# Kernel tuning notes

Hardware: AMD Instinct MI355X
Metric: run time of the kernel (lower is better)

## Reference

```python
import jax, jax.numpy as jnp
import numpy as np

N, T, H, W, C = 4, 8, 64, 64, 512
WS = 8  # window size; H, W are exact multiples so pad/depad are identity


def setup_inputs() -> dict:
    key = jax.random.key(0)
    k1, k2, k3, k4 = jax.random.split(key, 4)
    x = jax.random.normal(k1, (N, T, H, W, C), dtype=jnp.float32)
    local_pos_embed = jax.random.normal(k2, (WS, WS, C), dtype=jnp.float32)
    W_in = jax.random.normal(k3, (3 * C, C), dtype=jnp.float32) * 0.02
    b_in = jnp.zeros((3 * C,), dtype=jnp.float32)
    W_out = jax.random.normal(k4, (C, C), dtype=jnp.float32) * 0.02
    b_out = jnp.zeros((C,), dtype=jnp.float32)
    return {"x": x, "local_pos_embed": local_pos_embed, "W_in": W_in,
            "b_in": b_in, "W_out": W_out, "b_out": b_out, "num_heads": 8}


def reference(x, local_pos_embed, W_in, b_in, W_out, b_out, num_heads):
    n, t, h, w, c = x.shape
    ws = local_pos_embed.shape[0]
    nh, nw = h // ws, w // ws
    head_dim = c // num_heads
    scale = 1.0 / jnp.sqrt(jnp.asarray(head_dim, dtype=x.dtype))

    # window partition: (N*T, H, W, C) -> (N*T*nh*nw, ws*ws, C)
    xw = x.reshape(n * t, nh, ws, nw, ws, c)
    xw = xw.transpose(0, 1, 3, 2, 4, 5).reshape(n * t * nh * nw, ws * ws, c)

    pos = local_pos_embed.reshape(ws * ws, c)  # flatten(0,1)
    qk_in = xw + pos[None, :, :]               # pos added to q,k only

    Wq, Wk, Wv = W_in[:c], W_in[c:2 * c], W_in[2 * c:]
    bq, bk, bv = b_in[:c], b_in[c:2 * c], b_in[2 * c:]

    B, S = qk_in.shape[0], qk_in.shape[1]
    q = (qk_in @ Wq.T + bq).reshape(B, S, num_heads, head_dim)
    k = (qk_in @ Wk.T + bk).reshape(B, S, num_heads, head_dim)
    v = (xw @ Wv.T + bv).reshape(B, S, num_heads, head_dim)

    scores = jnp.einsum('bqhd,bkhd->bhqk', q * scale, k)
    attn = jax.nn.softmax(scores, axis=-1)
    out = jnp.einsum('bhqk,bkhd->bqhd', attn, v).reshape(B, S, c)
    out = out @ W_out.T + b_out

    # reverse window partition
    out = out.reshape(n * t, nh, nw, ws, ws, c)
    out = out.transpose(0, 1, 3, 2, 4, 5).reshape(n, t, h, w, c)
    return out
```

## Files before the change

kernel.cpp:

```cpp
#include <hip/hip_runtime.h>

typedef _Float16 f16;
typedef unsigned int u32;
typedef f16 f16x8 __attribute__((ext_vector_type(8)));
typedef f16 f16x4 __attribute__((ext_vector_type(4)));
typedef float f32x4 __attribute__((ext_vector_type(4)));


__device__ __forceinline__ int src_row(int m) {
    int win = m >> 6, s = m & 63;
    return ((win >> 6) << 12) | (((win >> 3) & 7) << 9) | ((s >> 3) << 6) |
           ((win & 7) << 3) | (s & 7);
}

__device__ __forceinline__ void gload_lds16(const void* g, void* lds) {
    __builtin_amdgcn_global_load_lds(
        (const __attribute__((address_space(1))) u32*)g,
        (__attribute__((address_space(3))) u32*)lds, 16, 0, 0);
}

__global__ __launch_bounds__(256) void prep_weights_k(
        const float* __restrict__ Wi, const float* __restrict__ Wo,
        f16* __restrict__ Wi_h, f16* __restrict__ Wo_h) {
    int i = blockIdx.x * 256 + threadIdx.x;
    const float4* src;
    f16* dst;
    int idx;
    if (i < 196608) { src = (const float4*)Wi; dst = Wi_h; idx = i; }
    else            { src = (const float4*)Wo; dst = Wo_h; idx = i - 196608; }
    float4 v = src[idx];
    f16x4 h = {(f16)v.x, (f16)v.y, (f16)v.z, (f16)v.w};
    *(f16x4*)(dst + (size_t)idx * 4) = h;
}

__global__ __launch_bounds__(256) void prep_bias_k(
        const float* __restrict__ pos, const float* __restrict__ Wi,
        const float* __restrict__ b_in, float* __restrict__ biasT) {
    int idx = blockIdx.x * 256 + threadIdx.x;
    int s = idx / 1536, o = idx % 1536;
    float acc = b_in[o];
    if (o < 1024) {
        const float4* p4 = (const float4*)(pos + (size_t)s * 512);
        const float4* w4 = (const float4*)(Wi + (size_t)o * 512);
        #pragma unroll 4
        for (int c = 0; c < 128; ++c) {
            float4 a = p4[c], b = w4[c];
            acc += a.x * b.x + a.y * b.y + a.z * b.z + a.w * b.w;
        }
    }
    biasT[idx] = acc;
}

__global__ __launch_bounds__(256) void prep_x_k(
        const float* __restrict__ x, f16* __restrict__ xh, int m0) {
    int i = blockIdx.x * 256 + threadIdx.x;
    int ml = i >> 6, c8 = (i & 63) * 8;
    int sr = src_row(m0 + ml);
    const float4* s4 = (const float4*)(x + (size_t)sr * 512 + c8);
    float4 a = s4[0], b = s4[1];
    f16x8 hv = {(f16)a.x, (f16)a.y, (f16)a.z, (f16)a.w,
                (f16)b.x, (f16)b.y, (f16)b.z, (f16)b.w};
    *(f16x8*)(xh + (size_t)ml * 512 + c8) = hv;
}

__global__ void __launch_bounds__(512, 2) qkv_gemm8_k(
        const f16* __restrict__ xh, const f16* __restrict__ Wh,
        const float* __restrict__ biasT, f16* __restrict__ qk,
        f16* __restrict__ vT, int nblk) {
    extern __shared__ f16 lds[];
    int tid = threadIdx.x;
    int lane = tid & 63, wid = tid >> 6;
    int l15 = lane & 15, g = lane >> 4;
    int wm = wid >> 2, wn = wid & 3;
    int sid = (blockIdx.x & 7) * (nblk >> 3) + (blockIdx.x >> 3);
    int bm = sid / 6, bn = sid % 6;
    const f16* Ap = xh + (size_t)bm * 256 * 512;
    const f16* Bp = Wh + (size_t)bn * 256 * 512;

    int li0 = tid, li1 = tid + 512;
    int r0 = li0 >> 3, c0 = li0 & 7, r1 = li1 >> 3, c1 = li1 & 7;
    int off0 = r0 * 512 + ((c0 ^ (r0 & 7)) * 8);
    int off1 = r1 * 512 + ((c1 ^ (r1 & 7)) * 8);

    auto stage = [&](const f16* panel, int ldsbase, int tt, int h) {
        int tb = tt & 1;
        int dst = ldsbase + (tb * 2 + h) * 8192 + wid * 512;
        const f16* src = panel + h * 65536 + tt * 64;
        gload_lds16(src + off0, (void*)&lds[dst]);
        gload_lds16(src + off1, (void*)&lds[dst + 4096]);
    };

    f32x4 acc[8][4];
    f32x4 zero4 = {0.f, 0.f, 0.f, 0.f};
    #pragma unroll
    for (int a = 0; a < 8; ++a)
        #pragma unroll
        for (int b = 0; b < 4; ++b) acc[a][b] = zero4;
    f16x8 bf[4][2];

    stage(Ap, 0, 0, 0); stage(Ap, 0, 0, 1);
    stage(Bp, 32768, 0, 0); stage(Bp, 32768, 0, 1);
    stage(Ap, 0, 1, 0); stage(Ap, 0, 1, 1);
    stage(Bp, 32768, 1, 0); stage(Bp, 32768, 1, 1);
    asm volatile("s_waitcnt vmcnt(0)" ::: "memory");
    __builtin_amdgcn_s_barrier();

    #pragma unroll
    for (int tt = 0; tt < 8; ++tt) {
        int tb = tt & 1;
        const f16* Ab = &lds[(tb * 2 + wm) * 8192];
        const f16* Bb = &lds[32768 + (tb * 2 + (wn >> 1)) * 8192];
        #pragma unroll
        for (int q = 0; q < 4; ++q) {
            f16x8 af[2][2];
            #pragma unroll
            for (int ml = 0; ml < 2; ++ml) {
                int rr = (q * 2 + ml) * 16 + l15;
                #pragma unroll
                for (int ks = 0; ks < 2; ++ks)
                    af[ml][ks] = *(const f16x8*)&Ab[rr * 64 + (((ks * 4 + g) ^ (rr & 7)) * 8)];
            }
            if (q == 0) {
                #pragma unroll
                for (int nf = 0; nf < 4; ++nf) {
                    int rb = (wn & 1) * 64 + nf * 16 + l15;
                    #pragma unroll
                    for (int ks = 0; ks < 2; ++ks)
                        bf[nf][ks] = *(const f16x8*)&Bb[rb * 64 + (((ks * 4 + g) ^ (rb & 7)) * 8)];
                }
            }
            if (q <= 1) {
                if ((tt & 1) ? (tt + 1 < 8) : (tt >= 2)) stage(Ap, 0, tt + 1, q);
            } else {
                if (tt + 2 < 8) stage(Bp, 32768, tt + 2, q - 2);
            }
            __builtin_amdgcn_s_barrier();
            __builtin_amdgcn_s_setprio(1);
            #pragma unroll
            for (int ml = 0; ml < 2; ++ml)
                #pragma unroll
                for (int nf = 0; nf < 4; ++nf)
                    #pragma unroll
                    for (int ks = 0; ks < 2; ++ks)
                        acc[q * 2 + ml][nf] = __builtin_amdgcn_mfma_f32_16x16x32_f16(
                            af[ml][ks], bf[nf][ks], acc[q * 2 + ml][nf], 0, 0, 0);
            __builtin_amdgcn_s_setprio(0);
            if (q == 3) {
                if (tt < 6)       asm volatile("s_waitcnt vmcnt(4)" ::: "memory");
                else if (tt == 6) asm volatile("s_waitcnt vmcnt(0)" ::: "memory");
            }
            __builtin_amdgcn_s_barrier();
        }
    }

    int browg = bm * 256 + wm * 128;
    if (bn < 4) {
        #pragma unroll
        for (int mf = 0; mf < 8; ++mf) {
            #pragma unroll
            for (int nf = 0; nf < 4; ++nf) {
                int col = bn * 256 + wn * 64 + nf * 16 + l15;
                #pragma unroll
                for (int j = 0; j < 4; ++j) {
                    int row = browg + mf * 16 + g * 4 + j;
                    float v = acc[mf][nf][j] + biasT[(row & 63) * 1536 + col];
                    qk[(size_t)row * 1024 + col] = (f16)v;
                }
            }
        }
    } else {
        __syncthreads();
        char* T = (char*)lds;
        int bn2 = bn - 4;
        #pragma unroll
        for (int mf = 0; mf < 8; ++mf) {
            #pragma unroll
            for (int nf = 0; nf < 4; ++nf) {
                int dl = wn * 64 + nf * 16 + l15;
                float bo = biasT[1024 + bn2 * 256 + dl];
                #pragma unroll
                for (int j = 0; j < 4; ++j) {
                    int sl = wm * 128 + mf * 16 + g * 4 + j;
                    *(f16*)(T + dl * 512 + ((sl * 2) ^ ((dl & 7) << 4))) =
                        (f16)(acc[mf][nf][j] + bo);
                }
            }
        }
        __syncthreads();
        #pragma unroll
        for (int r = 0; r < 16; ++r) {
            int c = r * 512 + tid;
            int dl = c >> 5, s0 = (c & 31) * 8;
            f16x8 v = *(const f16x8*)(T + dl * 512 + ((s0 * 2) ^ ((dl & 7) << 4)));
            int gcol = bn2 * 256 + dl;
            int head = gcol >> 6, dd = gcol & 63;
            int win = bm * 4 + (s0 >> 6);
            *(f16x8*)(vT + (size_t)win * 32768 + head * 4096 + dd * 64 + (s0 & 63)) = v;
        }
    }
}

__global__ __launch_bounds__(512) void attn_k(
        const f16* __restrict__ qk, const f16* __restrict__ vT,
        f16* __restrict__ attn_h) {
    __shared__ __align__(16) char S[64 * 1024];
    int tid = threadIdx.x;
    int lane = tid & 63, h = tid >> 6;
    int l15 = lane & 15, g = lane >> 4;
    const f16* baseqk = qk + (size_t)blockIdx.x * 64 * 1024;
    const f16* basev  = vT + (size_t)blockIdx.x * 32768 + h * 4096;
    int qc = h * 64, kc = 512 + h * 64;

    f32x4 zero4 = {0.f, 0.f, 0.f, 0.f};
    f32x4 acc[4][4];
    #pragma unroll
    for (int a = 0; a < 4; ++a)
        #pragma unroll
        for (int b = 0; b < 4; ++b) acc[a][b] = zero4;

    {
        f16x8 qf[4][2], kf[4][2];
        #pragma unroll
        for (int mf = 0; mf < 4; ++mf)
            #pragma unroll
            for (int ks = 0; ks < 2; ++ks)
                qf[mf][ks] = *reinterpret_cast<const f16x8*>(baseqk + (size_t)(mf * 16 + l15) * 1024 + qc + ks * 32 + g * 8);
        #pragma unroll
        for (int nf = 0; nf < 4; ++nf)
            #pragma unroll
            for (int ks = 0; ks < 2; ++ks)
                kf[nf][ks] = *reinterpret_cast<const f16x8*>(baseqk + (size_t)(nf * 16 + l15) * 1024 + kc + ks * 32 + g * 8);
        #pragma unroll
        for (int ks = 0; ks < 2; ++ks)
            #pragma unroll
            for (int mf = 0; mf < 4; ++mf)
                #pragma unroll
                for (int nf = 0; nf < 4; ++nf)
                    acc[mf][nf] = __builtin_amdgcn_mfma_f32_16x16x32_f16(qf[mf][ks], kf[nf][ks], acc[mf][nf], 0, 0, 0);
    }

    f16x8 vf[4][2];
    #pragma unroll
    for (int nf = 0; nf < 4; ++nf)
        #pragma unroll
        for (int ks = 0; ks < 2; ++ks)
            vf[nf][ks] = *reinterpret_cast<const f16x8*>(basev + (nf * 16 + l15) * 64 + ks * 32 + g * 8);

    char* Sh = S + h * 8192;
    #pragma unroll
    for (int mf = 0; mf < 4; ++mf) {
        #pragma unroll
        for (int j = 0; j < 4; ++j) {
            float mx = -1e30f;
            #pragma unroll
            for (int nf = 0; nf < 4; ++nf) mx = fmaxf(mx, acc[mf][nf][j]);
            #pragma unroll
            for (int off = 1; off < 16; off <<= 1) mx = fmaxf(mx, __shfl_xor(mx, off));
            float e[4], sum = 0.f;
            #pragma unroll
            for (int nf = 0; nf < 4; ++nf) {
                e[nf] = __expf((acc[mf][nf][j] - mx) * 0.125f);
                sum += e[nf];
            }
            #pragma unroll
            for (int off = 1; off < 16; off <<= 1) sum += __shfl_xor(sum, off);
            float rinv = __fdividef(1.0f, sum);
            int row = mf * 16 + g * 4 + j;
            #pragma unroll
            for (int nf = 0; nf < 4; ++nf)
                *(f16*)(Sh + row * 128 + (((nf * 16 + l15) * 2) ^ ((row & 7) << 4))) = (f16)(e[nf] * rinv);
        }
    }

    f32x4 acc2[4][4];
    #pragma unroll
    for (int a = 0; a < 4; ++a)
        #pragma unroll
        for (int b = 0; b < 4; ++b) acc2[a][b] = zero4;
    #pragma unroll
    for (int ks = 0; ks < 2; ++ks)
        #pragma unroll
        for (int mf = 0; mf < 4; ++mf) {
            int rr = mf * 16 + l15;
            f16x8 pa = *reinterpret_cast<const f16x8*>(Sh + rr * 128 + (((ks * 32 + g * 8) * 2) ^ ((rr & 7) << 4)));
            #pragma unroll
            for (int nf = 0; nf < 4; ++nf)
                acc2[mf][nf] = __builtin_amdgcn_mfma_f32_16x16x32_f16(pa, vf[nf][ks], acc2[mf][nf], 0, 0, 0);
        }

    f16* dst = attn_h + (size_t)blockIdx.x * 64 * 512 + h * 64;
    #pragma unroll
    for (int mf = 0; mf < 4; ++mf)
        #pragma unroll
        for (int nf = 0; nf < 4; ++nf)
            #pragma unroll
            for (int j = 0; j < 4; ++j)
                dst[(size_t)(mf * 16 + g * 4 + j) * 512 + nf * 16 + l15] = (f16)acc2[mf][nf][j];
}

__global__ void __launch_bounds__(512, 2) proj_gemm8_k(
        const f16* __restrict__ attn_h, const f16* __restrict__ Woh,
        const float* __restrict__ b_out, float* __restrict__ out, int nblk, int m0) {
    extern __shared__ f16 lds[];
    int tid = threadIdx.x;
    int lane = tid & 63, wid = tid >> 6;
    int l15 = lane & 15, g = lane >> 4;
    int wm = wid >> 2, wn = wid & 3;
    int sid = (blockIdx.x & 7) * (nblk >> 3) + (blockIdx.x >> 3);
    int bm = sid >> 1, bn = sid & 1;
    const f16* Ap = attn_h + (size_t)bm * 256 * 512;
    const f16* Bp = Woh + (size_t)bn * 256 * 512;

    int li0 = tid, li1 = tid + 512;
    int r0 = li0 >> 3, c0 = li0 & 7, r1 = li1 >> 3, c1 = li1 & 7;
    int off0 = r0 * 512 + ((c0 ^ (r0 & 7)) * 8);
    int off1 = r1 * 512 + ((c1 ^ (r1 & 7)) * 8);

    auto stage = [&](const f16* panel, int ldsbase, int tt, int h) {
        int tb = tt & 1;
        int dst = ldsbase + (tb * 2 + h) * 8192 + wid * 512;
        const f16* src = panel + h * 65536 + tt * 64;
        gload_lds16(src + off0, (void*)&lds[dst]);
        gload_lds16(src + off1, (void*)&lds[dst + 4096]);
    };

    f32x4 acc[8][4];
    f32x4 zero4 = {0.f, 0.f, 0.f, 0.f};
    #pragma unroll
    for (int a = 0; a < 8; ++a)
        #pragma unroll
        for (int b = 0; b < 4; ++b) acc[a][b] = zero4;
    f16x8 bf[4][2];

    stage(Ap, 0, 0, 0); stage(Ap, 0, 0, 1);
    stage(Bp, 32768, 0, 0); stage(Bp, 32768, 0, 1);
    stage(Ap, 0, 1, 0); stage(Ap, 0, 1, 1);
    stage(Bp, 32768, 1, 0); stage(Bp, 32768, 1, 1);
    asm volatile("s_waitcnt vmcnt(0)" ::: "memory");
    __builtin_amdgcn_s_barrier();

    #pragma unroll
    for (int tt = 0; tt < 8; ++tt) {
        int tb = tt & 1;
        const f16* Ab = &lds[(tb * 2 + wm) * 8192];
        const f16* Bb = &lds[32768 + (tb * 2 + (wn >> 1)) * 8192];
        #pragma unroll
        for (int q = 0; q < 4; ++q) {
            f16x8 af[2][2];
            #pragma unroll
            for (int ml = 0; ml < 2; ++ml) {
                int rr = (q * 2 + ml) * 16 + l15;
                #pragma unroll
                for (int ks = 0; ks < 2; ++ks)
                    af[ml][ks] = *(const f16x8*)&Ab[rr * 64 + (((ks * 4 + g) ^ (rr & 7)) * 8)];
            }
            if (q == 0) {
                #pragma unroll
                for (int nf = 0; nf < 4; ++nf) {
                    int rb = (wn & 1) * 64 + nf * 16 + l15;
                    #pragma unroll
                    for (int ks = 0; ks < 2; ++ks)
                        bf[nf][ks] = *(const f16x8*)&Bb[rb * 64 + (((ks * 4 + g) ^ (rb & 7)) * 8)];
                }
            }
            if (q <= 1) {
                if ((tt & 1) ? (tt + 1 < 8) : (tt >= 2)) stage(Ap, 0, tt + 1, q);
            } else {
                if (tt + 2 < 8) stage(Bp, 32768, tt + 2, q - 2);
            }
            __builtin_amdgcn_s_barrier();
            __builtin_amdgcn_s_setprio(1);
            #pragma unroll
            for (int ml = 0; ml < 2; ++ml)
                #pragma unroll
                for (int nf = 0; nf < 4; ++nf)
                    #pragma unroll
                    for (int ks = 0; ks < 2; ++ks)
                        acc[q * 2 + ml][nf] = __builtin_amdgcn_mfma_f32_16x16x32_f16(
                            af[ml][ks], bf[nf][ks], acc[q * 2 + ml][nf], 0, 0, 0);
            __builtin_amdgcn_s_setprio(0);
            if (q == 3) {
                if (tt < 6)       asm volatile("s_waitcnt vmcnt(4)" ::: "memory");
                else if (tt == 6) asm volatile("s_waitcnt vmcnt(0)" ::: "memory");
            }
            __builtin_amdgcn_s_barrier();
        }
    }

    int browg = bm * 256 + wm * 128, bcolg = bn * 256 + wn * 64;
    #pragma unroll
    for (int nf = 0; nf < 4; ++nf) {
        int col = bcolg + nf * 16 + l15;
        float bo = b_out[col];
        #pragma unroll
        for (int mf = 0; mf < 8; ++mf) {
            #pragma unroll
            for (int j = 0; j < 4; ++j) {
                int srow = src_row(m0 + browg + mf * 16 + g * 4 + j);
                out[(size_t)srow * 512 + col] = acc[mf][nf][j] + bo;
            }
        }
    }
}

extern "C" void kernel_launch(void* const* d_in, const int* in_sizes, int n_in,
                              void* d_out, int out_size, void* d_ws, size_t ws_size,
                              hipStream_t stream) {
    (void)in_sizes; (void)n_in; (void)out_size;
    const float* x     = (const float*)d_in[0];
    const float* pos   = (const float*)d_in[1];
    const float* W_in  = (const float*)d_in[2];
    const float* b_in  = (const float*)d_in[3];
    const float* W_out = (const float*)d_in[4];
    const float* b_out = (const float*)d_in[5];
    float* out = (float*)d_out;

    char* ws = (char*)d_ws;
    f16*   Wi_h  = (f16*)ws;
    f16*   Wo_h  = (f16*)(ws + 1572864);
    float* biasT = (float*)(ws + 2097152);
    const size_t fixed = 2490368;

    int chunks = 4;
    while (chunks < 64) {
        size_t need = fixed + ((size_t)131072 / chunks) * 4096;
        if (need <= ws_size) break;
        chunks <<= 1;
    }
    int Mc = 131072 / chunks;
    f16* xh = (f16*)(ws + fixed);
    f16* qk = (f16*)(ws + fixed + (size_t)Mc * 1024);
    f16* vT = (f16*)(ws + fixed + (size_t)Mc * 3072);
    int nblk  = (Mc / 256) * 6;
    int nblk2 = (Mc / 256) * 2;

    static_cast<void>(hipFuncSetAttribute((const void*)qkv_gemm8_k,
        hipFuncAttributeMaxDynamicSharedMemorySize, 131072));
    static_cast<void>(hipFuncSetAttribute((const void*)proj_gemm8_k,
        hipFuncAttributeMaxDynamicSharedMemorySize, 131072));

    prep_weights_k<<<1024, 256, 0, stream>>>(W_in, W_out, Wi_h, Wo_h);
    prep_bias_k<<<384, 256, 0, stream>>>(pos, W_in, b_in, biasT);
    for (int c = 0; c < chunks; ++c) {
        int m0 = c * Mc;
        prep_x_k<<<Mc / 4, 256, 0, stream>>>(x, xh, m0);
        qkv_gemm8_k<<<nblk, 512, 131072, stream>>>(xh, Wi_h, biasT, qk, vT, nblk);
        attn_k<<<Mc / 64, 512, 0, stream>>>(qk, vT, xh);
        proj_gemm8_k<<<nblk2, 512, 131072, stream>>>(xh, Wo_h, b_out, out, nblk2, m0);
    }
}
```

Measured before the change: 599.9 us.

## Stage GEMM/attention epilogues through LDS, transpose QK^T, relax prologue waits

The QKV GEMM epilogue and the attention output now go through swizzled LDS so that global stores are 16-byte vectors instead of scattered 2-byte writes. The attention score MFMA is transposed (K as the A operand), so each lane holds a query row's keys and softmax needs only two cross-lane shuffles instead of eight. The GEMM prologues wait with vmcnt(8) rather than 0 so the second tile's loads overlap the first tile's compute. The host starts with a single chunk to reduce the number of launches when workspace allows. These add extra barriers and LDS traffic in the epilogues.

```diff
diff --git a/kernel.cpp b/kernel.cpp
--- a/kernel.cpp
+++ b/kernel.cpp
@@ -102,7 +102,7 @@
     stage(Bp, 32768, 0, 0); stage(Bp, 32768, 0, 1);
     stage(Ap, 0, 1, 0); stage(Ap, 0, 1, 1);
     stage(Bp, 32768, 1, 0); stage(Bp, 32768, 1, 1);
-    asm volatile("s_waitcnt vmcnt(0)" ::: "memory");
+    asm volatile("s_waitcnt vmcnt(8)" ::: "memory");
     __builtin_amdgcn_s_barrier();
 
     #pragma unroll
@@ -156,17 +156,33 @@
     int browg = bm * 256 + wm * 128;
     if (bn < 4) {
         #pragma unroll
-        for (int mf = 0; mf < 8; ++mf) {
-            #pragma unroll
-            for (int nf = 0; nf < 4; ++nf) {
-                int col = bn * 256 + wn * 64 + nf * 16 + l15;
-                #pragma unroll
-                for (int j = 0; j < 4; ++j) {
-                    int row = browg + mf * 16 + g * 4 + j;
-                    float v = acc[mf][nf][j] + biasT[(row & 63) * 1536 + col];
-                    qk[(size_t)row * 1024 + col] = (f16)v;
+        for (int half = 0; half < 2; ++half) {
+            if (wm == half) {
+                #pragma unroll
+                for (int mf = 0; mf < 8; ++mf) {
+                    #pragma unroll
+                    for (int nf = 0; nf < 4; ++nf) {
+                        int col = bn * 256 + wn * 64 + nf * 16 + l15;
+                        int cloc = wn * 64 + nf * 16 + l15;
+                        #pragma unroll
+                        for (int j = 0; j < 4; ++j) {
+                            int r = mf * 16 + g * 4 + j;
+                            float v = acc[mf][nf][j] + biasT[(r & 63) * 1536 + col];
+                            *(f16*)((char*)lds + r * 512 + ((cloc * 2) ^ ((r & 7) << 4))) = (f16)v;
+                        }
+                    }
                 }
             }
+            __syncthreads();
+            int rowg0 = bm * 256 + half * 128;
+            #pragma unroll
+            for (int i = 0; i < 8; ++i) {
+                int c = i * 512 + tid;
+                int r = c >> 5, seg = c & 31;
+                f16x8 v = *(const f16x8*)((char*)lds + r * 512 + ((seg * 16) ^ ((r & 7) << 4)));
+                *(f16x8*)(qk + (size_t)(rowg0 + r) * 1024 + bn * 256 + seg * 8) = v;
+            }
+            __syncthreads();
         }
     } else {
         __syncthreads();
@@ -207,7 +223,7 @@
     int tid = threadIdx.x;
     int lane = tid & 63, h = tid >> 6;
     int l15 = lane & 15, g = lane >> 4;
-    const f16* baseqk = qk + (size_t)blockIdx.x * 64 * 1024;
+    const f16* baseqk = qk + (size_t)blockIdx.x * 65536;
     const f16* basev  = vT + (size_t)blockIdx.x * 32768 + h * 4096;
     int qc = h * 64, kc = 512 + h * 64;
 
@@ -233,10 +249,10 @@
         #pragma unroll
         for (int ks = 0; ks < 2; ++ks)
             #pragma unroll
-            for (int mf = 0; mf < 4; ++mf)
-                #pragma unroll
-                for (int nf = 0; nf < 4; ++nf)
-                    acc[mf][nf] = __builtin_amdgcn_mfma_f32_16x16x32_f16(qf[mf][ks], kf[nf][ks], acc[mf][nf], 0, 0, 0);
+            for (int ki = 0; ki < 4; ++ki)
+                #pragma unroll
+                for (int qi = 0; qi < 4; ++qi)
+                    acc[ki][qi] = __builtin_amdgcn_mfma_f32_16x16x32_f16(kf[ki][ks], qf[qi][ks], acc[ki][qi], 0, 0, 0);
     }
 
     f16x8 vf[4][2];
@@ -248,28 +264,34 @@
 
     char* Sh = S + h * 8192;
     #pragma unroll
-    for (int mf = 0; mf < 4; ++mf) {
-        #pragma unroll
-        for (int j = 0; j < 4; ++j) {
-            float mx = -1e30f;
-            #pragma unroll
-            for (int nf = 0; nf < 4; ++nf) mx = fmaxf(mx, acc[mf][nf][j]);
-            #pragma unroll
-            for (int off = 1; off < 16; off <<= 1) mx = fmaxf(mx, __shfl_xor(mx, off));
-            float e[4], sum = 0.f;
-            #pragma unroll
-            for (int nf = 0; nf < 4; ++nf) {
-                e[nf] = __expf((acc[mf][nf][j] - mx) * 0.125f);
-                sum += e[nf];
-            }
-            #pragma unroll
-            for (int off = 1; off < 16; off <<= 1) sum += __shfl_xor(sum, off);
-            float rinv = __fdividef(1.0f, sum);
-            int row = mf * 16 + g * 4 + j;
-            #pragma unroll
-            for (int nf = 0; nf < 4; ++nf)
-                *(f16*)(Sh + row * 128 + (((nf * 16 + l15) * 2) ^ ((row & 7) << 4))) = (f16)(e[nf] * rinv);
-        }
+    for (int qi = 0; qi < 4; ++qi) {
+        float mx = -1e30f;
+        #pragma unroll
+        for (int ki = 0; ki < 4; ++ki)
+            #pragma unroll
+            for (int j = 0; j < 4; ++j) mx = fmaxf(mx, acc[ki][qi][j]);
+        mx = fmaxf(mx, __shfl_xor(mx, 16));
+        mx = fmaxf(mx, __shfl_xor(mx, 32));
+        float sum = 0.f;
+        #pragma unroll
+        for (int ki = 0; ki < 4; ++ki)
+            #pragma unroll
+            for (int j = 0; j < 4; ++j) {
+                float e = __expf((acc[ki][qi][j] - mx) * 0.125f);
+                acc[ki][qi][j] = e;
+                sum += e;
+            }
+        sum += __shfl_xor(sum, 16);
+        sum += __shfl_xor(sum, 32);
+        float rinv = __fdividef(1.0f, sum);
+        int qrow = qi * 16 + l15;
+        char* rowp = Sh + qrow * 128;
+        int sw = (qrow & 7) << 4;
+        #pragma unroll
+        for (int ki = 0; ki < 4; ++ki)
+            #pragma unroll
+            for (int j = 0; j < 4; ++j)
+                *(f16*)(rowp + (((ki * 16 + g * 4 + j) * 2) ^ sw)) = (f16)(acc[ki][qi][j] * rinv);
     }
 
     f32x4 acc2[4][4];
@@ -288,14 +310,24 @@
                 acc2[mf][nf] = __builtin_amdgcn_mfma_f32_16x16x32_f16(pa, vf[nf][ks], acc2[mf][nf], 0, 0, 0);
         }
 
-    f16* dst = attn_h + (size_t)blockIdx.x * 64 * 512 + h * 64;
     #pragma unroll
     for (int mf = 0; mf < 4; ++mf)
         #pragma unroll
         for (int nf = 0; nf < 4; ++nf)
             #pragma unroll
-            for (int j = 0; j < 4; ++j)
-                dst[(size_t)(mf * 16 + g * 4 + j) * 512 + nf * 16 + l15] = (f16)acc2[mf][nf][j];
+            for (int j = 0; j < 4; ++j) {
+                int r = mf * 16 + g * 4 + j;
+                *(f16*)(Sh + r * 128 + (((nf * 16 + l15) * 2) ^ ((r & 7) << 4))) = (f16)acc2[mf][nf][j];
+            }
+    __syncthreads();
+    f16* dst = attn_h + (size_t)blockIdx.x * 32768;
+    #pragma unroll
+    for (int i = 0; i < 8; ++i) {
+        int c = i * 512 + tid;
+        int row = c >> 6, seg = c & 63;
+        f16x8 v = *(const f16x8*)(S + (seg >> 3) * 8192 + row * 128 + (((seg & 7) * 16) ^ ((row & 7) << 4)));
+        *(f16x8*)(dst + row * 512 + seg * 8) = v;
+    }
 }
 
 __global__ void __launch_bounds__(512, 2) proj_gemm8_k(
@@ -336,7 +368,7 @@
     stage(Bp, 32768, 0, 0); stage(Bp, 32768, 0, 1);
     stage(Ap, 0, 1, 0); stage(Ap, 0, 1, 1);
     stage(Bp, 32768, 1, 0); stage(Bp, 32768, 1, 1);
-    asm volatile("s_waitcnt vmcnt(0)" ::: "memory");
+    asm volatile("s_waitcnt vmcnt(8)" ::: "memory");
     __builtin_amdgcn_s_barrier();
 
     #pragma unroll
@@ -421,7 +453,7 @@
     float* biasT = (float*)(ws + 2097152);
     const size_t fixed = 2490368;
 
-    int chunks = 4;
+    int chunks = 1;
     while (chunks < 64) {
         size_t need = fixed + ((size_t)131072 / chunks) * 4096;
         if (need <= ws_size) break;
```

After: 603.4 us. No clear change (+0.6%).
